# Kernel tuning notes

Hardware: AMD Instinct MI355X
Metric: run time of the kernel (lower is better)

The kernel has to match this reference:

```python
import jax, jax.numpy as jnp
import numpy as np

H = 1024
S = 32768

def setup_inputs() -> dict:
    key = jax.random.key(0)
    k1, k2, k3, k4 = jax.random.split(key, 4)
    hidden = jax.random.normal(k1, (H,), dtype=jnp.float32)
    encoder_outputs = jax.random.normal(k2, (S, H), dtype=jnp.float32)
    W = jax.random.normal(k3, (H, H), dtype=jnp.float32) * (1.0 / np.sqrt(H))
    b = jax.random.normal(k4, (H,), dtype=jnp.float32) * 0.01
    return {"hidden": hidden, "encoder_outputs": encoder_outputs, "W": W, "b": b}

def reference(hidden, encoder_outputs, W, b):
    # energy_i = dot(hidden, W @ enc_i + b); vectorized over the seq dim.
    # [S,H] @ [H,H]^T -> [S,H]; then contract with hidden -> [S]
    energies = jnp.einsum('sh,h->s', encoder_outputs @ W.T + b, hidden)
    attn = jax.nn.softmax(energies)  # softmax over seq_len (dim 0), as in F.softmax
    return attn[None, None, :]  # [1, 1, S]
```

## Files before the change

### kernel.cpp

```cpp
#include <hip/hip_runtime.h>
#include <math.h>


#define H 1024
#define S 32768

__global__ __launch_bounds__(256) void k1_v_partial(const float* __restrict__ W,
                                                    const float* __restrict__ h,
                                                    float* __restrict__ partial_v) {
    __shared__ float lds[128];
    int ic   = blockIdx.x >> 3;
    int tile = blockIdx.x & 7;
    int t    = threadIdx.x;
    int c    = tile * 128 + (t & 127);
    int par  = t >> 7;
    int j0   = ic * 64 + par;
    float acc = 0.f;
    #pragma unroll 8
    for (int i = 0; i < 32; ++i) {
        int j = j0 + 2 * i;
        acc = fmaf(W[(size_t)j * H + c], h[j], acc);
    }
    if (par) lds[t - 128] = acc;
    __syncthreads();
    if (!par) partial_v[ic * H + c] = acc + lds[t];
}

__global__ __launch_bounds__(256) void k1b_v_reduce(const float* __restrict__ partial_v,
                                                    float* __restrict__ v,
                                                    float* __restrict__ sq) {
    __shared__ float lds[4];
    int t = threadIdx.x, lane = t & 63, wave = t >> 6;
    int c = blockIdx.x * 256 + t;
    float acc = 0.f;
    #pragma unroll
    for (int ic = 0; ic < 16; ++ic)
        acc += partial_v[ic * H + c];
    v[c] = acc;

    float q = acc * acc;
    #pragma unroll
    for (int off = 32; off; off >>= 1)
        q += __shfl_down(q, off, 64);
    if (lane == 0) lds[wave] = q;
    __syncthreads();
    if (t == 0)
        sq[blockIdx.x] = (lds[0] + lds[1]) + (lds[2] + lds[3]);
}

__global__ __launch_bounds__(256) void k2_energies(const float* __restrict__ E,
                                                   const float* __restrict__ v,
                                                   const float* __restrict__ sq,
                                                   float* __restrict__ out,
                                                   float* __restrict__ psum) {
    __shared__ float vl[H];
    __shared__ float red[16];
    int t = threadIdx.x;

    ((float4*)vl)[t] = ((const float4*)v)[t];
    float mm = 5.5f * sqrtf(((sq[0] + sq[1]) + (sq[2] + sq[3])));
    __syncthreads();

    int wave = t >> 6, lane = t & 63;
    const float4* v4 = (const float4*)vl;

    #pragma unroll 1
    for (int pair = 0; pair < 2; ++pair) {
        size_t row0 = (size_t)blockIdx.x * 16 + pair * 8 + wave * 2;
        const float4* e0 = (const float4*)(E + row0 * H);
        const float4* e1 = e0 + 256;

        float a0 = 0.f, a1 = 0.f;
        #pragma unroll
        for (int p = 0; p < 4; ++p) {
            float4 vv = v4[p * 64 + lane];
            float4 x0 = e0[p * 64 + lane];
            float4 x1 = e1[p * 64 + lane];
            a0 += x0.x * vv.x + x0.y * vv.y + x0.z * vv.z + x0.w * vv.w;
            a1 += x1.x * vv.x + x1.y * vv.y + x1.z * vv.z + x1.w * vv.w;
        }
        #pragma unroll
        for (int off = 32; off; off >>= 1) {
            a0 += __shfl_down(a0, off, 64);
            a1 += __shfl_down(a1, off, 64);
        }
        if (lane == 0) {
            float p0 = __expf(a0 - mm);
            float p1 = __expf(a1 - mm);
            *(float2*)(out + row0) = make_float2(p0, p1);
            red[pair * 8 + wave * 2]     = p0;
            red[pair * 8 + wave * 2 + 1] = p1;
        }
    }
    __syncthreads();
    if (t == 0) {
        float s = 0.f;
        #pragma unroll
        for (int i = 0; i < 16; ++i) s += red[i];
        psum[blockIdx.x] = s;
    }
}

__global__ __launch_bounds__(256) void k4_norm(float* __restrict__ out,
                                               const float* __restrict__ psum) {
    __shared__ float lds[4];
    int tid = threadIdx.x, lane = tid & 63, wave = tid >> 6;

    float a = 0.f;
    #pragma unroll 8
    for (int i = tid; i < 2048; i += 256)
        a += psum[i];
    #pragma unroll
    for (int off = 32; off; off >>= 1)
        a += __shfl_down(a, off, 64);
    if (lane == 0) lds[wave] = a;
    __syncthreads();
    float inv = 1.f / ((lds[0] + lds[1]) + (lds[2] + lds[3]));

    int s = blockIdx.x * 256 + tid;
    out[s] *= inv;
}

extern "C" void kernel_launch(void* const* d_in, const int* in_sizes, int n_in,
                              void* d_out, int out_size, void* d_ws, size_t ws_size,
                              hipStream_t stream) {
    const float* h = (const float*)d_in[0];
    const float* E = (const float*)d_in[1];
    const float* W = (const float*)d_in[2];
    float* out = (float*)d_out;
    float* ws  = (float*)d_ws;

    float* partial_v = ws;
    float* v         = ws + 16 * 1024;
    float* sq        = ws + 17 * 1024;
    float* psum      = ws + 17 * 1024 + 64;

    k1_v_partial<<<128,  256, 0, stream>>>(W, h, partial_v);
    k1b_v_reduce<<<4,    256, 0, stream>>>(partial_v, v, sq);
    k2_energies <<<2048, 256, 0, stream>>>(E, v, sq, out, psum);
    k4_norm     <<<128,  256, 0, stream>>>(out, psum);
}
```

Baseline: 35.93 us.

## Fuse v-reduction into k1 via last-block atomic and use nontemporal loads

Merges the separate v-reduce kernel into the partial-v kernel. A global atomic counter elects the last-finishing block, which sums the partials, writes v and precomputes the softmax max bound. This removes one kernel launch and its gap. The energies kernel also loads the large encoder matrix with nontemporal loads to avoid polluting cache. The counter is never reset but uses modulo 128, so it relies on the workspace starting at a multiple of 128. In exchange, the final reduction runs on a single block instead of four.

```diff
diff --git a/kernel.cpp b/kernel.cpp
--- a/kernel.cpp
+++ b/kernel.cpp
@@ -5,10 +5,17 @@
 #define H 1024
 #define S 32768
 
-__global__ __launch_bounds__(256) void k1_v_partial(const float* __restrict__ W,
-                                                    const float* __restrict__ h,
-                                                    float* __restrict__ partial_v) {
+typedef float f4 __attribute__((ext_vector_type(4)));
+
+__global__ __launch_bounds__(256) void k1_fused(const float* __restrict__ W,
+                                                const float* __restrict__ h,
+                                                float* __restrict__ partial_v,
+                                                float* __restrict__ v,
+                                                float* __restrict__ m0,
+                                                unsigned int* __restrict__ ctr) {
     __shared__ float lds[128];
+    __shared__ float l2[4];
+    __shared__ int last_flag;
     int ic   = blockIdx.x >> 3;
     int tile = blockIdx.x & 7;
     int t    = threadIdx.x;
@@ -24,33 +31,41 @@
     if (par) lds[t - 128] = acc;
     __syncthreads();
     if (!par) partial_v[ic * H + c] = acc + lds[t];
-}
 
-__global__ __launch_bounds__(256) void k1b_v_reduce(const float* __restrict__ partial_v,
-                                                    float* __restrict__ v,
-                                                    float* __restrict__ sq) {
-    __shared__ float lds[4];
-    int t = threadIdx.x, lane = t & 63, wave = t >> 6;
-    int c = blockIdx.x * 256 + t;
-    float acc = 0.f;
+    __syncthreads();
+    if (t == 0) {
+        __threadfence();
+        unsigned int old = __hip_atomic_fetch_add(ctr, 1u, __ATOMIC_ACQ_REL,
+                                                  __HIP_MEMORY_SCOPE_AGENT);
+        last_flag = ((old & 127u) == 127u);
+    }
+    __syncthreads();
+    if (!last_flag) return;
+
+    float sq_acc = 0.f;
     #pragma unroll
-    for (int ic = 0; ic < 16; ++ic)
-        acc += partial_v[ic * H + c];
-    v[c] = acc;
-
-    float q = acc * acc;
+    for (int rep = 0; rep < 4; ++rep) {
+        int cc = rep * 256 + t;
+        float a = 0.f;
+        #pragma unroll
+        for (int icx = 0; icx < 16; ++icx)
+            a += partial_v[icx * H + cc];
+        v[cc] = a;
+        sq_acc += a * a;
+    }
+    int lane = t & 63, wave = t >> 6;
     #pragma unroll
     for (int off = 32; off; off >>= 1)
-        q += __shfl_down(q, off, 64);
-    if (lane == 0) lds[wave] = q;
+        sq_acc += __shfl_down(sq_acc, off, 64);
+    if (lane == 0) l2[wave] = sq_acc;
     __syncthreads();
     if (t == 0)
-        sq[blockIdx.x] = (lds[0] + lds[1]) + (lds[2] + lds[3]);
+        m0[0] = 5.5f * sqrtf((l2[0] + l2[1]) + (l2[2] + l2[3]));
 }
 
 __global__ __launch_bounds__(256) void k2_energies(const float* __restrict__ E,
                                                    const float* __restrict__ v,
-                                                   const float* __restrict__ sq,
+                                                   const float* __restrict__ m0,
                                                    float* __restrict__ out,
                                                    float* __restrict__ psum) {
     __shared__ float vl[H];
@@ -58,26 +73,27 @@
     int t = threadIdx.x;
 
     ((float4*)vl)[t] = ((const float4*)v)[t];
-    float mm = 5.5f * sqrtf(((sq[0] + sq[1]) + (sq[2] + sq[3])));
+    float mm = m0[0];
     __syncthreads();
 
     int wave = t >> 6, lane = t & 63;
-    const float4* v4 = (const float4*)vl;
+    const f4* v4 = (const f4*)vl;
 
     #pragma unroll 1
     for (int pair = 0; pair < 2; ++pair) {
         size_t row0 = (size_t)blockIdx.x * 16 + pair * 8 + wave * 2;
-        const float4* e0 = (const float4*)(E + row0 * H);
-        const float4* e1 = e0 + 256;
+        const f4* e0 = (const f4*)(E + row0 * H);
+        const f4* e1 = e0 + 256;
 
         float a0 = 0.f, a1 = 0.f;
         #pragma unroll
         for (int p = 0; p < 4; ++p) {
-            float4 vv = v4[p * 64 + lane];
-            float4 x0 = e0[p * 64 + lane];
-            float4 x1 = e1[p * 64 + lane];
-            a0 += x0.x * vv.x + x0.y * vv.y + x0.z * vv.z + x0.w * vv.w;
-            a1 += x1.x * vv.x + x1.y * vv.y + x1.z * vv.z + x1.w * vv.w;
+            int idx = p * 64 + lane;
+            f4 vv = v4[idx];
+            f4 x0 = __builtin_nontemporal_load(e0 + idx);
+            f4 x1 = __builtin_nontemporal_load(e1 + idx);
+            a0 += x0[0] * vv[0] + x0[1] * vv[1] + x0[2] * vv[2] + x0[3] * vv[3];
+            a1 += x1[0] * vv[0] + x1[1] * vv[1] + x1[2] * vv[2] + x1[3] * vv[3];
         }
         #pragma unroll
         for (int off = 32; off; off >>= 1) {
@@ -130,13 +146,13 @@
     float* out = (float*)d_out;
     float* ws  = (float*)d_ws;
 
-    float* partial_v = ws;
-    float* v         = ws + 16 * 1024;
-    float* sq        = ws + 17 * 1024;
-    float* psum      = ws + 17 * 1024 + 64;
+    float* partial_v  = ws;
+    float* v          = ws + 16 * 1024;
+    float* m0         = ws + 17 * 1024;
+    unsigned int* ctr = (unsigned int*)(ws + 17 * 1024 + 64);
+    float* psum       = ws + 17 * 1024 + 128;
 
-    k1_v_partial<<<128,  256, 0, stream>>>(W, h, partial_v);
-    k1b_v_reduce<<<4,    256, 0, stream>>>(partial_v, v, sq);
-    k2_energies <<<2048, 256, 0, stream>>>(E, v, sq, out, psum);
-    k4_norm     <<<128,  256, 0, stream>>>(out, psum);
+    k1_fused   <<<128,  256, 0, stream>>>(W, h, partial_v, v, m0, ctr);
+    k2_energies<<<2048, 256, 0, stream>>>(E, v, m0, out, psum);
+    k4_norm    <<<128,  256, 0, stream>>>(out, psum);
 }
```

Result: no change. 36.12 us (+0.5%).

## Double-buffer encoder rows into LDS via async global_load_lds in energies kernel

Applied to the files above, without the earlier changes.

The energies kernel now streams each wave's four encoder rows through a per-wave double buffer in shared memory, using direct global-to-LDS loads and explicit vmcnt waits so the next row's load overlaps the current row's dot product. The attention vector v is kept in registers instead of being staged through shared memory, and the block barrier before compute is removed. This adds 32KB of LDS per block, which may lower occupancy, and relies on hand-placed wait counts being correct.

```diff
diff --git a/kernel.cpp b/kernel.cpp
--- a/kernel.cpp
+++ b/kernel.cpp
@@ -4,6 +4,14 @@
 
 #define H 1024
 #define S 32768
+
+typedef float f4 __attribute__((ext_vector_type(4)));
+typedef __attribute__((address_space(1))) void* gas1_t;
+typedef __attribute__((address_space(3))) void* gas3_t;
+
+__device__ __forceinline__ float dot4(f4 a, f4 b) {
+    return a[0] * b[0] + a[1] * b[1] + a[2] * b[2] + a[3] * b[3];
+}
 
 __global__ __launch_bounds__(256) void k1_v_partial(const float* __restrict__ W,
                                                     const float* __restrict__ h,
@@ -53,52 +61,74 @@
                                                    const float* __restrict__ sq,
                                                    float* __restrict__ out,
                                                    float* __restrict__ psum) {
-    __shared__ float vl[H];
-    __shared__ float red[16];
-    int t = threadIdx.x;
+    __shared__ __align__(16) float stage[4][2][1024];
+    __shared__ float red[4];
+    int t = threadIdx.x, wave = t >> 6, lane = t & 63;
 
-    ((float4*)vl)[t] = ((const float4*)v)[t];
-    float mm = 5.5f * sqrtf(((sq[0] + sq[1]) + (sq[2] + sq[3])));
+    const f4* V4 = (const f4*)v;
+    f4 vr0 = V4[lane];
+    f4 vr1 = V4[64 + lane];
+    f4 vr2 = V4[128 + lane];
+    f4 vr3 = V4[192 + lane];
+    float mm = 5.5f * sqrtf((sq[0] + sq[1]) + (sq[2] + sq[3]));
+
+    size_t rowbase = (size_t)blockIdx.x * 16 + wave * 4;
+    const f4* g = (const f4*)(E + rowbase * H);
+    float* st0 = &stage[wave][0][0];
+    float* st1 = &stage[wave][1][0];
+
+    #define ISSUE(buf, r) do {                                                  \
+        __builtin_amdgcn_global_load_lds((gas1_t)(g + (r) * 256 +       lane),  \
+                                         (gas3_t)((buf)),        16, 0, 0);     \
+        __builtin_amdgcn_global_load_lds((gas1_t)(g + (r) * 256 +  64 + lane),  \
+                                         (gas3_t)((buf) +  256), 16, 0, 0);     \
+        __builtin_amdgcn_global_load_lds((gas1_t)(g + (r) * 256 + 128 + lane),  \
+                                         (gas3_t)((buf) +  512), 16, 0, 0);     \
+        __builtin_amdgcn_global_load_lds((gas1_t)(g + (r) * 256 + 192 + lane),  \
+                                         (gas3_t)((buf) +  768), 16, 0, 0);     \
+    } while (0)
+
+    #define CONSUME(buf, ri) do {                                               \
+        const f4* sb = (const f4*)(buf);                                        \
+        f4 x0 = sb[lane];                                                       \
+        f4 x1 = sb[64 + lane];                                                  \
+        f4 x2 = sb[128 + lane];                                                 \
+        f4 x3 = sb[192 + lane];                                                 \
+        float a = dot4(x0, vr0) + dot4(x1, vr1);                                \
+        a      += dot4(x2, vr2) + dot4(x3, vr3);                                \
+        _Pragma("unroll")                                                       \
+        for (int off = 32; off; off >>= 1)                                      \
+            a += __shfl_down(a, off, 64);                                       \
+        if (lane == 0) {                                                        \
+            float p = __expf(a - mm);                                           \
+            out[rowbase + (ri)] = p;                                            \
+            wsum += p;                                                          \
+        }                                                                       \
+    } while (0)
+
+    float wsum = 0.f;
+
+    ISSUE(st0, 0);
+    ISSUE(st1, 1);
+    asm volatile("s_waitcnt vmcnt(4)" ::: "memory");
+    __builtin_amdgcn_sched_barrier(0);
+    CONSUME(st0, 0);
+    ISSUE(st0, 2);
+    asm volatile("s_waitcnt vmcnt(4)" ::: "memory");
+    __builtin_amdgcn_sched_barrier(0);
+    CONSUME(st1, 1);
+    ISSUE(st1, 3);
+    asm volatile("s_waitcnt vmcnt(4)" ::: "memory");
+    __builtin_amdgcn_sched_barrier(0);
+    CONSUME(st0, 2);
+    asm volatile("s_waitcnt vmcnt(0)" ::: "memory");
+    __builtin_amdgcn_sched_barrier(0);
+    CONSUME(st1, 3);
+
+    if (lane == 0) red[wave] = wsum;
     __syncthreads();
-
-    int wave = t >> 6, lane = t & 63;
-    const float4* v4 = (const float4*)vl;
-
-    #pragma unroll 1
-    for (int pair = 0; pair < 2; ++pair) {
-        size_t row0 = (size_t)blockIdx.x * 16 + pair * 8 + wave * 2;
-        const float4* e0 = (const float4*)(E + row0 * H);
-        const float4* e1 = e0 + 256;
-
-        float a0 = 0.f, a1 = 0.f;
-        #pragma unroll
-        for (int p = 0; p < 4; ++p) {
-            float4 vv = v4[p * 64 + lane];
-            float4 x0 = e0[p * 64 + lane];
-            float4 x1 = e1[p * 64 + lane];
-            a0 += x0.x * vv.x + x0.y * vv.y + x0.z * vv.z + x0.w * vv.w;
-            a1 += x1.x * vv.x + x1.y * vv.y + x1.z * vv.z + x1.w * vv.w;
-        }
-        #pragma unroll
-        for (int off = 32; off; off >>= 1) {
-            a0 += __shfl_down(a0, off, 64);
-            a1 += __shfl_down(a1, off, 64);
-        }
-        if (lane == 0) {
-            float p0 = __expf(a0 - mm);
-            float p1 = __expf(a1 - mm);
-            *(float2*)(out + row0) = make_float2(p0, p1);
-            red[pair * 8 + wave * 2]     = p0;
-            red[pair * 8 + wave * 2 + 1] = p1;
-        }
-    }
-    __syncthreads();
-    if (t == 0) {
-        float s = 0.f;
-        #pragma unroll
-        for (int i = 0; i < 16; ++i) s += red[i];
-        psum[blockIdx.x] = s;
-    }
+    if (t == 0)
+        psum[blockIdx.x] = (red[0] + red[1]) + (red[2] + red[3]);
 }
 
 __global__ __launch_bounds__(256) void k4_norm(float* __restrict__ out,
```

Measured after the change: 36.36 us. No clear change (+1.2%).
